# Optimization experiments

Measured on AMD Instinct MI355X. Metric: run time of the kernel, lower is better.

Reference implementation:

```python
import jax, jax.numpy as jnp
import numpy as np

SELECT_NUM = 5
N_OBJ = 256


def conv(x, w, b, stride=1, pad=None):
    """NCHW conv. pad=None -> VALID; pad=1 -> [(1,1),(1,1)]."""
    padding = 'VALID' if pad is None else [(pad, pad), (pad, pad)]
    out = jax.lax.conv_general_dilated(
        x, w, (stride, stride), padding,
        dimension_numbers=('NCHW', 'OIHW', 'NCHW'))
    return out + b[None, :, None, None]


def setup_inputs() -> dict:
    key = jax.random.key(0)
    ks = jax.random.split(key, 20)

    def p(k, shape, fan_in):
        return (jax.random.normal(k, shape, jnp.float32) / np.float32(np.sqrt(fan_in)))

    inp = {}
    inp['glob_feature'] = jax.random.normal(ks[0], (1, 1024, 28, 28), jnp.float32)
    inp['roi_features'] = jax.random.normal(ks[1], (N_OBJ, 2048, 7, 7), jnp.float32)
    # valid boxes in a 1280x720 image: x1>x0, y1>y0 so log(.) is finite
    x0 = jax.random.uniform(ks[2], (N_OBJ,), minval=0.0, maxval=600.0)
    y0 = jax.random.uniform(ks[3], (N_OBJ,), minval=0.0, maxval=340.0)
    x1 = x0 + jax.random.uniform(ks[4], (N_OBJ,), minval=10.0, maxval=600.0)
    y1 = y0 + jax.random.uniform(ks[5], (N_OBJ,), minval=10.0, maxval=340.0)
    inp['bbox'] = jnp.stack([x0, y0, x1, y1], axis=1)

    # global branch
    inp['w_glob1'] = p(ks[6], (512, 1024, 4, 4), 1024 * 16); inp['b_glob1'] = jnp.zeros(512, jnp.float32)
    inp['w_glob2'] = p(ks[7], (256, 512, 4, 4), 512 * 16);   inp['b_glob2'] = jnp.zeros(256, jnp.float32)
    # object branch
    inp['w_obj1'] = p(ks[8], (1024, 2048, 3, 3), 2048 * 9);  inp['b_obj1'] = jnp.zeros(1024, jnp.float32)
    inp['w_obj2'] = p(ks[9], (256, 1024, 3, 3), 1024 * 9);   inp['b_obj2'] = jnp.zeros(256, jnp.float32)
    # selector (516 = 260 obj + 256 glob)
    inp['w_sel1'] = p(ks[10], (256, 516, 3, 3), 516 * 9);    inp['b_sel1'] = jnp.zeros(256, jnp.float32)
    inp['w_sel2'] = p(ks[11], (16, 256, 3, 3), 256 * 9);     inp['b_sel2'] = jnp.zeros(16, jnp.float32)
    inp['w_sel3'] = p(ks[12], (1, 16, 3, 3), 16 * 9);        inp['b_sel3'] = jnp.zeros(1, jnp.float32)
    # FC head (eval mode: dropout = identity)
    inp['w_fc1'] = p(ks[13], (516, 256), 516);               inp['b_fc1'] = jnp.zeros(256, jnp.float32)
    inp['w_fc2'] = p(ks[14], (256 * SELECT_NUM, 64), 1280);  inp['b_fc2'] = jnp.zeros(64, jnp.float32)
    inp['w_fc3'] = p(ks[15], (64, 4), 64);                   inp['b_fc3'] = jnp.zeros(4, jnp.float32)
    return inp


def reference(glob_feature, roi_features, bbox,
              w_glob1, b_glob1, w_glob2, b_glob2,
              w_obj1, b_obj1, w_obj2, b_obj2,
              w_sel1, b_sel1, w_sel2, b_sel2, w_sel3, b_sel3,
              w_fc1, b_fc1, w_fc2, b_fc2, w_fc3, b_fc3):
    # global branch: [1,1024,28,28] -> [1,512,14,14] -> [1,256,7,7]; pool(7) is identity
    glob = jax.nn.relu(conv(glob_feature, w_glob1, b_glob1, stride=2, pad=1))
    glob = jax.nn.relu(conv(glob, w_glob2, b_glob2, stride=2, pad=1))

    # object branch: [N,2048,7,7] -> [N,1024,7,7] -> [N,256,7,7]
    obj = jax.nn.relu(conv(roi_features, w_obj1, b_obj1, pad=1))
    obj = jax.nn.relu(conv(obj, w_obj2, b_obj2, pad=1))

    # bbox normalization (uses original coords; image is 1280x720)
    x0, y0, x1, y1 = bbox[:, 0], bbox[:, 1], bbox[:, 2], bbox[:, 3]
    bb = jnp.stack([x0 / 1280.0, y0 / 720.0,
                    jnp.log(1280.0 / (x1 - x0)),
                    jnp.log(720.0 / (y1 - y0))], axis=1)  # [N,4]
    bb = jnp.broadcast_to(bb[:, :, None, None], (bb.shape[0], 4, 7, 7))
    obj = jnp.concatenate([bb, obj], axis=1)  # [N,260,7,7]

    # selector: concat with broadcast glob, 3 valid convs 7->5->3->1
    glob2 = jnp.broadcast_to(glob, (obj.shape[0], 256, 7, 7))
    s = jnp.concatenate([obj, glob2], axis=1)  # [N,516,7,7]
    s = jax.nn.relu(conv(s, w_sel1, b_sel1))
    s = jax.nn.relu(conv(s, w_sel2, b_sel2))
    s = conv(s, w_sel3, b_sel3).reshape(-1)  # [N]

    # top-k selection (sort descending over objects)
    idx = jnp.argsort(-s)[:SELECT_NUM]
    obj = obj[idx] / np.float32(SELECT_NUM)  # [5,260,7,7]

    # adaptive avg pool to 1x1 == mean over HW
    obj = obj.mean(axis=(2, 3))                               # [5,260]
    g = jnp.broadcast_to(glob.mean(axis=(2, 3)), (SELECT_NUM, 256))  # [5,256]
    x = jnp.concatenate([obj, g], axis=1)                     # [5,516]

    x = jax.nn.relu(x @ w_fc1 + b_fc1)   # dropout is identity in eval
    tmp = x.reshape(-1)                  # [1280]
    x = jax.nn.relu(tmp @ w_fc2 + b_fc2) # [64]
    x = x @ w_fc3 + b_fc3                # [4]
    return x
```

## Files before the change

kernel.cpp:

```cpp
#include <hip/hip_runtime.h>
#include <math.h>

using half8 = __attribute__((ext_vector_type(8))) _Float16;
using half4 = __attribute__((ext_vector_type(4))) _Float16;
using f32x4 = __attribute__((ext_vector_type(4))) float;

template<int CIN, int KC, int M_, int BM>
__global__ __launch_bounds__(256)
void transform_w(const float* __restrict__ w, _Float16* __restrict__ wt) {
  constexpr int NT = (KC / 32) * 9;
  __shared__ float lds[32 * 289];
  const int tid = threadIdx.x;
  const int s   = blockIdx.x;
  const int m0  = blockIdx.y * 32;
  const int ci0 = s * 32;
  int vlen = (CIN - ci0) * 9;
  if (vlen > 288) vlen = 288;
  if (vlen < 0) vlen = 0;

  for (int e = tid; e < 32 * 288; e += 256) {
    const int mi = e / 288, o = e - mi * 288;
    float v = 0.f;
    if (o < vlen) v = w[(size_t)(m0 + mi) * (CIN * 9) + (size_t)ci0 * 9 + o];
    lds[mi * 289 + o] = v;
  }
  __syncthreads();

  const int cc  = s >> 2;
  const int sub = s & 3;
  int ns = (KC - 128 * cc) / 32; if (ns > 4) ns = 4;
  const int mt = m0 / BM;
  const int mb = m0 - mt * BM;
  _Float16* base = wt + (size_t)mt * NT * (BM * 32);

  for (int u = tid; u < 36 * 256; u += 256) {
    const int chunk  = u >> 8;
    const int within = u & 255;
    const int g = chunk & 3, khkw = chunk >> 2;
    const int mi = within >> 3, i = within & 7;
    const int kt = 36 * cc + khkw * ns + sub;
    const float v = lds[mi * 289 + (8 * g + i) * 9 + khkw];
    base[(size_t)kt * (BM * 32) + g * (BM * 8) + (mb + mi) * 8 + i] = (_Float16)v;
  }
}

__global__ __launch_bounds__(256)
void convert_tr(const float* __restrict__ x, _Float16* __restrict__ xh) {
  __shared__ _Float16 t_s[49][136];
  const int tid   = threadIdx.x;
  const int cbase = blockIdx.x * 128;
  const int obj   = blockIdx.y;
  const float* src = x + (size_t)obj * 2048 * 49 + (size_t)cbase * 49;
  for (int e = tid; e < 128 * 49; e += 256) {
    const int ci = e / 49, pos = e - ci * 49;
    t_s[pos][ci] = (_Float16)src[e];
  }
  __syncthreads();
  _Float16* dst = xh + (size_t)obj * 49 * 2048 + cbase;
  for (int u = tid; u < 49 * 16; u += 256) {
    const int pos = u >> 4, l = u & 15;
    *(half8*)&dst[(size_t)pos * 2048 + l * 8] = *(const half8*)&t_s[pos][l * 8];
  }
}

template<int KC, int BM, int FN, int OHW, int PAD, bool TOUT, typename OUT_T,
         int NMT, int NOP>
__global__ __launch_bounds__(512)
void conv_mfma(const _Float16* __restrict__ Wt, const _Float16* __restrict__ X,
               const float* __restrict__ bias, OUT_T* __restrict__ out,
               int outc, int co_off) {
  constexpr int NT    = (KC / 32) * 9;
  constexpr int OPOS  = OHW * OHW;
  constexpr int WM    = BM / 4;
  constexpr int FR    = WM / 16;
  constexpr int CFULL = KC / 128;
  constexpr int TAIL  = KC - CFULL * 128;
  constexpr int NCH   = CFULL + (TAIL ? 1 : 0);

  __shared__ alignas(16) _Float16 x_s[2][50][136];

  const int tid  = threadIdx.x;
  const int wid  = tid >> 6;
  const int lane = tid & 63;
  const int g    = lane >> 4;
  const int ln   = lane & 15;
  const int obj  = wid >> 2;
  const int wm   = (wid & 3) * WM;

  const int bid = blockIdx.x;
  const int j = bid & 7, q = bid >> 3;
  constexpr int OPJ = 8 / NMT;
  const int mt = j / OPJ;
  const int op = (j % OPJ) * (NOP / OPJ) + q;

// ... 27 lines not shown
          const int row = u >> 4, l = u & 15;
          const int o = row >= 49 ? 1 : 0, pos = row - 49 * o;
          rg[v] = *(const half8*)(Xh + (size_t)(o * 49 + pos) * KC + cbase + l * 8);
        }
      }
    } else {
      if (tid < 392) {
        const int row = tid >> 2, l = tid & 3;
        const int o = row >= 49 ? 1 : 0, pos = row - 49 * o;
        rg[0] = *(const half8*)(Xh + (size_t)(o * 49 + pos) * KC + cbase + l * 8);
      }
    }
  };
  auto write_chunk = [&](int cw) {
    if (cw == 128) {
#pragma unroll
      for (int v = 0; v < 4; v++) {
        const int u = v * 512 + tid;
        if (u < 1568) {
          const int row = u >> 4, l = u & 15;
          const int o = row >= 49 ? 1 : 0, pos = row - 49 * o;
          *(half8*)&x_s[o][pos][l * 8] = rg[v];
        }
      }
    } else {
      if (tid < 392) {
        const int row = tid >> 2, l = tid & 3;
        const int o = row >= 49 ? 1 : 0, pos = row - 49 * o;
        *(half8*)&x_s[o][pos][l * 8] = rg[0];
      }
    }
  };

  const int afoff = (g * BM + wm + ln) * 8;
  const _Float16* ap = Wt + (size_t)mt * NT * (BM * 32) + afoff;
  half8 afA[FR], afB[FR], afC[FR];
#pragma unroll
  for (int r = 0; r < FR; r++) afA[r] = *(const half8*)(ap + r * 128);
  ap += BM * 32;
#pragma unroll
  for (int r = 0; r < FR; r++) afB[r] = *(const half8*)(ap + r * 128);
  ap += BM * 32;

  load_chunk(0, KC < 128 ? KC : 128);

  auto kstep = [&](half8 (&cur)[FR], half8 (&fut)[FR], int subbyte,
                   const int (&boff)[FN]) {
#pragma unroll
    for (int r = 0; r < FR; r++) fut[r] = *(const half8*)(ap + r * 128);
    ap += BM * 32;
    __builtin_amdgcn_s_setprio(1);
    const char* xb = (const char*)(&x_s[0][0][0]) + subbyte;
#pragma unroll
    for (int f = 0; f < FN; f++) {
      const half8 bf = *(const half8*)(xb + boff[f]);
#pragma unroll
      for (int r = 0; r < FR; r++)
        acc[r][f] = __builtin_amdgcn_mfma_f32_16x16x32_f16(cur[r], bf, acc[r][f], 0, 0, 0);
    }
    __builtin_amdgcn_s_setprio(0);
  };

  for (int c = 0; c < NCH; c++) {
    const int cw = (c < CFULL) ? 128 : TAIL;
    asm volatile("s_barrier" ::: "memory");
    write_chunk(cw);
    if (c + 1 < NCH)
      load_chunk((c + 1) * 128, (c + 1 < CFULL) ? 128 : TAIL);
    asm volatile("s_waitcnt lgkmcnt(0)\n\ts_barrier" ::: "memory");

    if (cw == 128) {
#pragma unroll
      for (int t9 = 0; t9 < 9; t9++) {
        const int kh = t9 / 3, kw = t9 - 3 * (t9 / 3);
        int boff[FN];
#pragma unroll
        for (int f = 0; f < FN; f++) {
          const int ih = ohv[f] + kh - PAD;
          const int iw = owv[f] + kw - PAD;
          bool v = pvv[f];
          if (PAD) v = v && ((unsigned)ih < 7u) && ((unsigned)iw < 7u);
          const int row = v ? (ih * 7 + iw) : 49;
          boff[f] = (obj * 50 * 136 + row * 136) * 2;
        }
#pragma unroll
        for (int s4 = 0; s4 < 4; s4++) {
          const int ph = (t9 * 4 + s4) % 3;
          const int subbyte = (s4 * 32 + 8 * g) * 2;
          if (ph == 0)      kstep(afA, afC, subbyte, boff);
          else if (ph == 1) kstep(afB, afA, subbyte, boff);
          else              kstep(afC, afB, subbyte, boff);
        }
      }
    } else {
#pragma unroll
      for (int t9 = 0; t9 < 9; t9++) {
        const int kh = t9 / 3, kw = t9 - 3 * (t9 / 3);
        int boff[FN];
#pragma unroll
        for (int f = 0; f < FN; f++) {
          const int ih = ohv[f] + kh - PAD;
          const int iw = owv[f] + kw - PAD;
          bool v = pvv[f];
          if (PAD) v = v && ((unsigned)ih < 7u) && ((unsigned)iw < 7u);
          const int row = v ? (ih * 7 + iw) : 49;
          boff[f] = (obj * 50 * 136 + row * 136) * 2;
        }
        const int ph = t9 % 3;
        const int subbyte = (8 * g) * 2;
        if (ph == 0)      kstep(afA, afC, subbyte, boff);
        else if (ph == 1) kstep(afB, afA, subbyte, boff);
        else              kstep(afC, afB, subbyte, boff);
      }
    }
  }

  if constexpr (TOUT) {
    __shared__ alignas(16) _Float16 ot_s[2][49][132];
    constexpr int PASSES = BM / 128;
#pragma unroll
    for (int p = 0; p < PASSES; p++) {
      if (p) asm volatile("s_barrier" ::: "memory");
      if (wm >= 128 * p && wm < 128 * (p + 1)) {
#pragma unroll
        for (int f = 0; f < FN; f++) {
          const int pos = ln + 16 * f;
          if (pos < OPOS) {
#pragma unroll
            for (int r = 0; r < FR; r++) {
              const int cl = wm - 128 * p + r * 16 + g * 4;
              half4 h;
#pragma unroll
              for (int e = 0; e < 4; e++)
                h[e] = (_Float16)fmaxf(
                    acc[r][f][e] + bias[mt * BM + wm + r * 16 + g * 4 + e], 0.f);
              *(half4*)&ot_s[obj][pos][cl] = h;
            }
          }
        }
      }
      asm volatile("s_waitcnt lgkmcnt(0)\n\ts_barrier" ::: "memory");
      _Float16* dst = (_Float16*)out;
      for (int u = tid; u < 2 * 49 * 32; u += 512) {
        const int row = u >> 5, l = u & 31;
        const int o = row >= 49 ? 1 : 0, pos = row - 49 * o;
        const half4 v = *(const half4*)&ot_s[o][pos][l * 4];
        *(half4*)&dst[((size_t)(2 * op + o) * OPOS + pos) * outc +
                      co_off + mt * BM + 128 * p + l * 4] = v;
      }
    }
  } else {
    const int bo = 2 * op + obj;
#pragma unroll
    for (int f = 0; f < FN; f++) {
      const int pos = ln + 16 * f;
      if (pos < OPOS) {
#pragma unroll
        for (int r = 0; r < FR; r++) {
          const int mrow = mt * BM + wm + r * 16 + g * 4;
#pragma unroll
          for (int e = 0; e < 4; e++) {
            const int m = mrow + e;
            float v = fmaxf(acc[r][f][e] + bias[m], 0.f);
            out[((size_t)bo * outc + co_off + m) * OPOS + pos] = (OUT_T)v;
          }
        }
      }
    }
  }
}

template<int M_, int CIN, int KH, int KW, int H, int W, int OH, int OW,
         int STRIDE, int PAD, int BATCH, int OUTC, int CO_OFF, bool RELU,
         int TM, int TN, int KSPLIT, bool PARTIAL>
__global__ __launch_bounds__(256)
void conv_gemm(const float* __restrict__ A,
               const float* __restrict__ X,
               const float* __restrict__ bias,
               float* __restrict__ out) {
  constexpr int K   = CIN * KH * KW;
  constexpr int N   = BATCH * OH * OW;
  constexpr int BK  = 16;
  constexpr int BM  = 16 * TM;
  constexpr int BN  = 16 * TN;
  constexpr int KCH = K / KSPLIT;

  __shared__ float a_s[BK][BM];
  __shared__ float b_s[BK][BN];

  const int t  = threadIdx.x;
  const int tx = t & 15;
  const int ty = t >> 4;
  const int n0 = blockIdx.x * BN;
  const int m0 = blockIdx.y * BM;
  const int kz = blockIdx.z;

  constexpr int AQ    = TM / 4;
  constexpr int TPR_A = 4 / AQ;
  const int am = t / TPR_A;
  const int ak = (t % TPR_A) * (4 * AQ);

  constexpr int BQ = TN / 4;
  const int bk = t & 15;
  const int bn = (t >> 4) * TN;

  float acc[TM][TN];
#pragma unroll
  for (int i = 0; i < TM; i++)
#pragma unroll
    for (int j = 0; j < TN; j++) acc[i][j] = 0.f;

  for (int k0 = kz * KCH; k0 < (kz + 1) * KCH; k0 += BK) {
    float4 av[AQ];
#pragma unroll
    for (int q = 0; q < AQ; q++) {
      av[q] = make_float4(0.f, 0.f, 0.f, 0.f);
      const int kq = k0 + ak + 4 * q;
      if ((m0 + am) < M_ && kq < K)
        av[q] = *reinterpret_cast<const float4*>(&A[(m0 + am) * K + kq]);
    }
    float bv[TN];
#pragma unroll
    for (int q = 0; q < TN; q++) bv[q] = 0.f;
    {
      const int kk = k0 + bk;
      if (kk < K) {
        const int ci = kk / (KH * KW);
        const int r  = kk - ci * (KH * KW);
        const int kh = r / KW;
        const int kw = r - kh * KW;
#pragma unroll
        for (int q = 0; q < TN; q++) {
          const int n = n0 + bn + q;
          if (n < N) {
            const int b   = n / (OH * OW);
            const int pos = n - b * (OH * OW);
            const int oh  = pos / OW;
            const int ow  = pos - oh * OW;
            const int ih  = oh * STRIDE - PAD + kh;
            const int iw  = ow * STRIDE - PAD + kw;
            if (ih >= 0 && ih < H && iw >= 0 && iw < W)
              bv[q] = X[((b * CIN + ci) * H + ih) * W + iw];
          }
        }
      }
    }
    __syncthreads();
#pragma unroll
    for (int q = 0; q < AQ; q++) {
      const int kq = ak + 4 * q;
      a_s[kq + 0][am] = av[q].x;
      a_s[kq + 1][am] = av[q].y;
      a_s[kq + 2][am] = av[q].z;
      a_s[kq + 3][am] = av[q].w;
    }
#pragma unroll
    for (int q = 0; q < BQ; q++)
      *reinterpret_cast<float4*>(&b_s[bk][bn + 4 * q]) =
          make_float4(bv[4 * q], bv[4 * q + 1], bv[4 * q + 2], bv[4 * q + 3]);
    __syncthreads();
#pragma unroll
    for (int kk2 = 0; kk2 < BK; kk2++) {
      float a[TM], b[TN];
#pragma unroll
      for (int q = 0; q < AQ; q++)
        *reinterpret_cast<float4*>(&a[4 * q]) =
            *reinterpret_cast<const float4*>(&a_s[kk2][ty * TM + 4 * q]);
#pragma unroll
      for (int q = 0; q < BQ; q++)
        *reinterpret_cast<float4*>(&b[4 * q]) =
            *reinterpret_cast<const float4*>(&b_s[kk2][tx * TN + 4 * q]);
#pragma unroll
      for (int i = 0; i < TM; i++)
#pragma unroll
        for (int j = 0; j < TN; j++)
          acc[i][j] = fmaf(a[i], b[j], acc[i][j]);
    }
  }

#pragma unroll
  for (int i = 0; i < TM; i++) {
    const int m = m0 + ty * TM + i;
    if (m < M_) {
#pragma unroll
      for (int j = 0; j < TN; j++) {
        const int n = n0 + tx * TN + j;
        if (n < N) {
          if (PARTIAL) {
            out[((size_t)kz * M_ + m) * N + n] = acc[i][j];
          } else {
            float v = acc[i][j] + bias[m];
            if (RELU) v = fmaxf(v, 0.f);
            const int b   = n / (OH * OW);
            const int pos = n - b * (OH * OW);
            out[(b * OUTC + CO_OFF + m) * (OH * OW) + pos] = v;
          }
        }
      }
    }
  }
}

__global__ void reduce_bias_relu(const float* __restrict__ part,
                                 const float* __restrict__ bias,
                                 float* __restrict__ out, int MN, int N, int KS) {
  const int e = blockIdx.x * 256 + threadIdx.x;
  if (e >= MN) return;
  float s = 0.f;
  for (int k = 0; k < KS; k++) s += part[(size_t)k * MN + e];
  s += bias[e / N];
  out[e] = fmaxf(s, 0.f);
}

__global__ __launch_bounds__(256)
void sel2_kernel(const float* __restrict__ x, const float* __restrict__ w,
                 const float* __restrict__ b, float* __restrict__ out) {
  const int wv   = (blockIdx.x * 256 + threadIdx.x) >> 6;
  const int lane = threadIdx.x & 63;
  const int obj  = wv >> 4, co = wv & 15;
  float acc[9];
#pragma unroll
  for (int p = 0; p < 9; p++) acc[p] = 0.f;
  const float* xo = x + (size_t)obj * 256 * 25;
  const float* wo = w + (size_t)co * 2304;
  for (int k = lane; k < 2304; k += 64) {
    const int ci = k / 9, rr = k - 9 * ci;
    const int kh = rr / 3, kw = rr - 3 * kh;
    const float wval = wo[k];
    const float* xc = xo + ci * 25;
#pragma unroll
    for (int oh = 0; oh < 3; oh++)
#pragma unroll
      for (int ow = 0; ow < 3; ow++)
        acc[oh * 3 + ow] = fmaf(xc[(oh + kh) * 5 + (ow + kw)], wval, acc[oh * 3 + ow]);
  }
  const float bv = b[co];
#pragma unroll
  for (int p = 0; p < 9; p++) {
    float v = acc[p];
#pragma unroll
    for (int off = 32; off; off >>= 1) v += __shfl_xor(v, off);
    if (lane == 0) out[(size_t)wv * 9 + p] = fmaxf(v + bv, 0.f);
  }
}

__global__ void prep_sin_t(const float* __restrict__ bbox,
                           const float* __restrict__ glob,
                           _Float16* __restrict__ sint) {
  const int b = blockIdx.x;
  const float x0 = bbox[b * 4 + 0], y0 = bbox[b * 4 + 1];
  const float x1 = bbox[b * 4 + 2], y1 = bbox[b * 4 + 3];
  const float bbv[4] = {x0 / 1280.f, y0 / 720.f,
                        logf(1280.f / (x1 - x0)), logf(720.f / (y1 - y0))};
  _Float16* base = sint + (size_t)b * 49 * 544;
  for (int e = threadIdx.x; e < 49 * 288; e += blockDim.x) {
    const int pos = e / 288, q = e - pos * 288;
    float v; int c;
    if (q < 4)        { v = bbv[q];                  c = q; }
    else if (q < 260) { v = glob[(q - 4) * 49 + pos]; c = q + 256; }
    else              { v = 0.f;                      c = q + 256; }
    base[pos * 544 + c] = (_Float16)v;
  }
}

__global__ void score_top5(const float* __restrict__ sel2,
                           const float* __restrict__ w3,
                           const float* __restrict__ b3,
                           int* __restrict__ idx_out) {
  __shared__ float w_s[144];
  __shared__ float s_s[256];
  const int t = threadIdx.x;
  if (t < 144) w_s[t] = w3[t];
  __syncthreads();
  float acc = b3[0];
  const float* p = sel2 + t * 144;
  for (int k = 0; k < 144; k++) acc += p[k] * w_s[k];
  s_s[t] = acc;
  __syncthreads();
  if (t == 0) {
    for (int i = 0; i < 5; i++) {
      float best = -1e30f;
      int bi = 0;
      for (int j = 0; j < 256; j++)
        if (s_s[j] > best) { best = s_s[j]; bi = j; }
      idx_out[i] = bi;
      s_s[bi] = -1e30f;
    }
  }
}

__global__ void pool_t(const _Float16* __restrict__ sint,
                       const float* __restrict__ glob,
                       const int* __restrict__ idx,
                       float* __restrict__ objsel,
                       float* __restrict__ g) {
  const int blk = blockIdx.x;
  const int t = threadIdx.x;
  if (blk < 5) {
    const int b = idx[blk];
    const _Float16* base = sint + (size_t)b * 49 * 544;
    for (int c = t; c < 260; c += blockDim.x) {
      float s = 0.f;
      for (int p = 0; p < 49; p++) s += (float)base[p * 544 + c];
      objsel[blk * 260 + c] = s * (1.f / 245.f);
    }
  } else {
    if (t < 256) {
      float s = 0.f;
      const float* p = glob + t * 49;
      for (int q = 0; q < 49; q++) s += p[q];
      g[t] = s * (1.f / 49.f);
    }
  }
}

__global__ void fc1_kernel(const float* __restrict__ objsel,
                           const float* __restrict__ g,
                           const float* __restrict__ w,
                           const float* __restrict__ b,
                           float* __restrict__ x1) {
  const int co = threadIdx.x;
  float acc[5];
#pragma unroll
  for (int i = 0; i < 5; i++) acc[i] = b[co];
  for (int k = 0; k < 260; k++) {
    const float wv = w[k * 256 + co];
#pragma unroll
    for (int i = 0; i < 5; i++) acc[i] = fmaf(objsel[i * 260 + k], wv, acc[i]);
  }
  for (int k = 260; k < 516; k++) {
    const float wv = w[k * 256 + co];
    const float gv = g[k - 260];
#pragma unroll
    for (int i = 0; i < 5; i++) acc[i] = fmaf(gv, wv, acc[i]);
  }
#pragma unroll
  for (int i = 0; i < 5; i++) x1[i * 256 + co] = fmaxf(acc[i], 0.f);
}

__global__ void fc23_kernel(const float* __restrict__ x1,
                            const float* __restrict__ w2,
                            const float* __restrict__ b2,
                            const float* __restrict__ w3,
                            const float* __restrict__ b3,
                            float* __restrict__ out) {
  __shared__ float x2[64];
  const int j = threadIdx.x;
  float acc = b2[j];
  for (int k = 0; k < 1280; k++) acc = fmaf(x1[k], w2[k * 64 + j], acc);
  x2[j] = fmaxf(acc, 0.f);
  __syncthreads();
  if (j < 4) {
    float a = b3[j];
    for (int k = 0; k < 64; k++) a = fmaf(x2[k], w3[k * 4 + j], a);
    out[j] = a;
  }
}

extern "C" void kernel_launch(void* const* d_in, const int* in_sizes, int n_in,
                              void* d_out, int out_size, void* d_ws, size_t ws_size,
                              hipStream_t stream) {
  (void)in_sizes; (void)n_in; (void)out_size; (void)ws_size;
  const float* glob_feature = (const float*)d_in[0];
  const float* roi          = (const float*)d_in[1];
  const float* bbox         = (const float*)d_in[2];
  const float* w_glob1      = (const float*)d_in[3];
  const float* b_glob1      = (const float*)d_in[4];
  const float* w_glob2      = (const float*)d_in[5];
  const float* b_glob2      = (const float*)d_in[6];
  const float* w_obj1       = (const float*)d_in[7];
  const float* b_obj1       = (const float*)d_in[8];
  const float* w_obj2       = (const float*)d_in[9];
  const float* b_obj2       = (const float*)d_in[10];
  const float* w_sel1       = (const float*)d_in[11];
  const float* b_sel1       = (const float*)d_in[12];
  const float* w_sel2       = (const float*)d_in[13];
  const float* b_sel2       = (const float*)d_in[14];
  const float* w_sel3       = (const float*)d_in[15];
  const float* b_sel3       = (const float*)d_in[16];
  const float* w_fc1        = (const float*)d_in[17];
  const float* b_fc1        = (const float*)d_in[18];
  const float* w_fc2        = (const float*)d_in[19];
  const float* b_fc2        = (const float*)d_in[20];
  const float* w_fc3        = (const float*)d_in[21];
  const float* b_fc3        = (const float*)d_in[22];

  float* ws = (float*)d_ws;
  _Float16* xh1     = (_Float16*)(ws);
  _Float16* wbuf1   = (_Float16*)(ws + 12845056);
  _Float16* obj1buf = (_Float16*)(ws + 22282240);
  _Float16* sint    = (_Float16*)(ws);
  _Float16* wbuf2   = (_Float16*)(ws + 3411968);
  _Float16* wbufs1  = (_Float16*)(ws + 4591616);
  float*    sel1buf = ws + 5218304;
  float*    glob1buf= ws + 6856704;
  float*    part1   = ws + 6957056;
  float*    part2   = ws + 8562688;
  float*    sel2buf = ws + 8763392;
  float*    globbuf = ws + 8800256;
  int*      idxbuf  = (int*)(ws + 8812800);
  float*    objsel  = ws + 8812808;
  float*    gbuf    = ws + 8814108;
  float*    x1buf   = ws + 8814364;

  transform_w<2048, 2048, 1024, 256><<<dim3(64, 32), 256, 0, stream>>>(w_obj1, wbuf1);
  convert_tr<<<dim3(16, 256), 256, 0, stream>>>(roi, xh1);
  conv_mfma<2048, 256, 4, 7, 1, true, _Float16, 4, 128>
      <<<dim3(512), 512, 0, stream>>>(wbuf1, xh1, b_obj1, obj1buf, 1024, 0);

  transform_w<1024, 1024, 256, 128><<<dim3(32, 8), 256, 0, stream>>>(w_obj2, wbuf2);
  transform_w<516, 544, 256, 128><<<dim3(17, 8), 256, 0, stream>>>(w_sel1, wbufs1);

  conv_gemm<512, 1024, 4, 4, 28, 28, 14, 14, 2, 1, 1, 512, 0, true, 4, 4, 16, true>
      <<<dim3(4, 8, 16), 256, 0, stream>>>(w_glob1, glob_feature, b_glob1, part1);
  reduce_bias_relu<<<dim3(392), 256, 0, stream>>>(part1, b_glob1, glob1buf, 100352, 196, 16);
  conv_gemm<256, 512, 4, 4, 14, 14, 7, 7, 2, 1, 1, 256, 0, true, 4, 4, 16, true>
      <<<dim3(1, 4, 16), 256, 0, stream>>>(w_glob2, glob1buf, b_glob2, part2);
  reduce_bias_relu<<<dim3(49), 256, 0, stream>>>(part2, b_glob2, globbuf, 12544, 49, 16);

  prep_sin_t<<<dim3(256), 256, 0, stream>>>(bbox, globbuf, sint);

  conv_mfma<1024, 128, 4, 7, 1, true, _Float16, 2, 128>
      <<<dim3(256), 512, 0, stream>>>(wbuf2, obj1buf, b_obj2, sint, 544, 4);
  conv_mfma<544, 128, 2, 5, 0, false, float, 2, 128>
      <<<dim3(256), 512, 0, stream>>>(wbufs1, sint, b_sel1, sel1buf, 256, 0);
  sel2_kernel<<<dim3(1024), 256, 0, stream>>>(sel1buf, w_sel2, b_sel2, sel2buf);
  score_top5<<<dim3(1), 256, 0, stream>>>(sel2buf, w_sel3, b_sel3, idxbuf);

  pool_t<<<dim3(6), 256, 0, stream>>>(sint, globbuf, idxbuf, objsel, gbuf);
  fc1_kernel<<<dim3(1), 256, 0, stream>>>(objsel, gbuf, w_fc1, b_fc1, x1buf);
  fc23_kernel<<<dim3(1), 64, 0, stream>>>(x1buf, w_fc2, b_fc2, w_fc3, b_fc3,
                                          (float*)d_out);
}
```

Baseline: 991.6 us.

## Merge prep kernels, retile obj1 conv with 8 waves, fuse FC head

Combines the weight transform and input transpose into one prep launch, and the obj2/sel1 weight transforms plus the glob1 conv into a second launch. It adds a new conv_mfma2 for the big obj1 conv with BM=512, 8 waves along M, and FN=7 covering both objects, so each block does more work. The score, top-5, pooling and FC layers are fused into one head kernel. This cuts launch overhead and is meant to improve weight reuse, at the cost of more registers per block and different occupancy.

```diff
diff --git a/kernel.cpp b/kernel.cpp
--- a/kernel.cpp
+++ b/kernel.cpp
@@ -6,18 +6,13 @@
 using f32x4 = __attribute__((ext_vector_type(4))) float;
 
 template<int CIN, int KC, int M_, int BM>
-__global__ __launch_bounds__(256)
-void transform_w(const float* __restrict__ w, _Float16* __restrict__ wt) {
+__device__ void transform_w_dev(float* lds, const float* __restrict__ w,
+                                _Float16* __restrict__ wt, int s, int m0, int tid) {
   constexpr int NT = (KC / 32) * 9;
-  __shared__ float lds[32 * 289];
-  const int tid = threadIdx.x;
-  const int s   = blockIdx.x;
-  const int m0  = blockIdx.y * 32;
   const int ci0 = s * 32;
   int vlen = (CIN - ci0) * 9;
   if (vlen > 288) vlen = 288;
   if (vlen < 0) vlen = 0;
-
   for (int e = tid; e < 32 * 288; e += 256) {
     const int mi = e / 288, o = e - mi * 288;
     float v = 0.f;
@@ -25,17 +20,13 @@
     lds[mi * 289 + o] = v;
   }
   __syncthreads();
-
-  const int cc  = s >> 2;
-  const int sub = s & 3;
+  const int cc = s >> 2, sub = s & 3;
   int ns = (KC - 128 * cc) / 32; if (ns > 4) ns = 4;
   const int mt = m0 / BM;
   const int mb = m0 - mt * BM;
   _Float16* base = wt + (size_t)mt * NT * (BM * 32);
-
   for (int u = tid; u < 36 * 256; u += 256) {
-    const int chunk  = u >> 8;
-    const int within = u & 255;
+    const int chunk = u >> 8, within = u & 255;
     const int g = chunk & 3, khkw = chunk >> 2;
     const int mi = within >> 3, i = within & 7;
     const int kt = 36 * cc + khkw * ns + sub;
@@ -44,12 +35,9 @@
   }
 }
 
-__global__ __launch_bounds__(256)
-void convert_tr(const float* __restrict__ x, _Float16* __restrict__ xh) {
-  __shared__ _Float16 t_s[49][136];
-  const int tid   = threadIdx.x;
-  const int cbase = blockIdx.x * 128;
-  const int obj   = blockIdx.y;
+__device__ void convert_tr_dev(_Float16 (*t_s)[136], const float* __restrict__ x,
+                               _Float16* __restrict__ xh, int cb, int obj, int tid) {
+  const int cbase = cb * 128;
   const float* src = x + (size_t)obj * 2048 * 49 + (size_t)cbase * 49;
   for (int e = tid; e < 128 * 49; e += 256) {
     const int ci = e / 49, pos = e - ci * 49;
@@ -60,6 +48,346 @@
   for (int u = tid; u < 49 * 16; u += 256) {
     const int pos = u >> 4, l = u & 15;
     *(half8*)&dst[(size_t)pos * 2048 + l * 8] = *(const half8*)&t_s[pos][l * 8];
+  }
+}
+
+template<int M_, int CIN, int KH, int KW, int H, int W, int OH, int OW,
+         int STRIDE, int PAD, int BATCH, int OUTC, int CO_OFF, bool RELU,
+         int TM, int TN, int KSPLIT, bool PARTIAL>
+__device__ void conv_gemm_dev(char* shraw, const float* __restrict__ A,
+                              const float* __restrict__ X,
+                              const float* __restrict__ bias,
+                              float* __restrict__ out,
+                              int n0, int m0, int kz, int t) {
+  constexpr int K   = CIN * KH * KW;
+  constexpr int N   = BATCH * OH * OW;
+  constexpr int BK  = 16;
+  constexpr int BM  = 16 * TM;
+  constexpr int BN  = 16 * TN;
+  constexpr int KCH = K / KSPLIT;
+
+  float (*a_s)[BM] = (float (*)[BM])shraw;
+  float (*b_s)[BN] = (float (*)[BN])(shraw + sizeof(float) * BK * BM);
+
+  const int tx = t & 15;
+  const int ty = t >> 4;
+  constexpr int AQ    = TM / 4;
+  constexpr int TPR_A = 4 / AQ;
+  const int am = t / TPR_A;
+  const int ak = (t % TPR_A) * (4 * AQ);
+  constexpr int BQ = TN / 4;
+  const int bk = t & 15;
+  const int bn = (t >> 4) * TN;
+
+  float acc[TM][TN];
+#pragma unroll
+  for (int i = 0; i < TM; i++)
+#pragma unroll
+    for (int j = 0; j < TN; j++) acc[i][j] = 0.f;
+
+  for (int k0 = kz * KCH; k0 < (kz + 1) * KCH; k0 += BK) {
+    float4 av[AQ];
+#pragma unroll
+    for (int q = 0; q < AQ; q++) {
+      av[q] = make_float4(0.f, 0.f, 0.f, 0.f);
+      const int kq = k0 + ak + 4 * q;
+      if ((m0 + am) < M_ && kq < K)
+        av[q] = *reinterpret_cast<const float4*>(&A[(m0 + am) * K + kq]);
+    }
+    float bv[TN];
+#pragma unroll
+    for (int q = 0; q < TN; q++) bv[q] = 0.f;
+    {
+      const int kk = k0 + bk;
+      if (kk < K) {
+        const int ci = kk / (KH * KW);
+        const int r  = kk - ci * (KH * KW);
+        const int kh = r / KW;
+        const int kw = r - kh * KW;
+#pragma unroll
+        for (int q = 0; q < TN; q++) {
+          const int n = n0 + bn + q;
+          if (n < N) {
+            const int b   = n / (OH * OW);
+            const int pos = n - b * (OH * OW);
+            const int oh  = pos / OW;
+            const int ow  = pos - oh * OW;
+            const int ih  = oh * STRIDE - PAD + kh;
+            const int iw  = ow * STRIDE - PAD + kw;
+            if (ih >= 0 && ih < H && iw >= 0 && iw < W)
+              bv[q] = X[((b * CIN + ci) * H + ih) * W + iw];
+          }
+        }
+      }
+    }
+    __syncthreads();
+#pragma unroll
+    for (int q = 0; q < AQ; q++) {
+      const int kq = ak + 4 * q;
+      a_s[kq + 0][am] = av[q].x;
+      a_s[kq + 1][am] = av[q].y;
+      a_s[kq + 2][am] = av[q].z;
+      a_s[kq + 3][am] = av[q].w;
+    }
+#pragma unroll
+    for (int q = 0; q < BQ; q++)
+      *reinterpret_cast<float4*>(&b_s[bk][bn + 4 * q]) =
+          make_float4(bv[4 * q], bv[4 * q + 1], bv[4 * q + 2], bv[4 * q + 3]);
+    __syncthreads();
+#pragma unroll
+    for (int kk2 = 0; kk2 < BK; kk2++) {
+      float a[TM], b[TN];
+#pragma unroll
+      for (int q = 0; q < AQ; q++)
+        *reinterpret_cast<float4*>(&a[4 * q]) =
+            *reinterpret_cast<const float4*>(&a_s[kk2][ty * TM + 4 * q]);
+#pragma unroll
+      for (int q = 0; q < BQ; q++)
+        *reinterpret_cast<float4*>(&b[4 * q]) =
+            *reinterpret_cast<const float4*>(&b_s[kk2][tx * TN + 4 * q]);
+#pragma unroll
+      for (int i = 0; i < TM; i++)
+#pragma unroll
+        for (int j = 0; j < TN; j++)
+          acc[i][j] = fmaf(a[i], b[j], acc[i][j]);
+    }
+  }
+
+#pragma unroll
+  for (int i = 0; i < TM; i++) {
+    const int m = m0 + ty * TM + i;
+    if (m < M_) {
+#pragma unroll
+      for (int j = 0; j < TN; j++) {
+        const int n = n0 + tx * TN + j;
+        if (n < N) {
+          if (PARTIAL) {
+            out[((size_t)kz * M_ + m) * N + n] = acc[i][j];
+          } else {
+            float v = acc[i][j] + bias[m];
+            if (RELU) v = fmaxf(v, 0.f);
+            const int b   = n / (OH * OW);
+            const int pos = n - b * (OH * OW);
+            out[(b * OUTC + CO_OFF + m) * (OH * OW) + pos] = v;
+          }
+        }
+      }
+    }
+  }
+}
+
+template<int M_, int CIN, int KH, int KW, int H, int W, int OH, int OW,
+         int STRIDE, int PAD, int BATCH, int OUTC, int CO_OFF, bool RELU,
+         int TM, int TN, int KSPLIT, bool PARTIAL>
+__global__ __launch_bounds__(256)
+void conv_gemm(const float* __restrict__ A, const float* __restrict__ X,
+               const float* __restrict__ bias, float* __restrict__ out) {
+  __shared__ char sh[16 * (16 * TM + 16 * TN) * 4];
+  conv_gemm_dev<M_, CIN, KH, KW, H, W, OH, OW, STRIDE, PAD, BATCH, OUTC, CO_OFF,
+                RELU, TM, TN, KSPLIT, PARTIAL>(
+      sh, A, X, bias, out, blockIdx.x * 16 * TN, blockIdx.y * 16 * TM,
+      blockIdx.z, threadIdx.x);
+}
+
+__global__ __launch_bounds__(256)
+void prep1(const float* __restrict__ w_obj1, _Float16* __restrict__ wbuf1,
+           const float* __restrict__ roi, _Float16* __restrict__ xh1) {
+  __shared__ char sh[32 * 289 * 4];
+  int b = blockIdx.x;
+  if (b < 2048) {
+    transform_w_dev<2048, 2048, 1024, 512>((float*)sh, w_obj1, wbuf1,
+                                           b & 63, (b >> 6) * 32, threadIdx.x);
+  } else {
+    b -= 2048;
+    convert_tr_dev((_Float16(*)[136])sh, roi, xh1, b & 15, b >> 4, threadIdx.x);
+  }
+}
+
+__global__ __launch_bounds__(256)
+void prep2(const float* __restrict__ w_obj2, _Float16* __restrict__ wbuf2,
+           const float* __restrict__ w_sel1, _Float16* __restrict__ wbufs1,
+           const float* __restrict__ w_glob1, const float* __restrict__ gfeat,
+           float* __restrict__ part1) {
+  __shared__ char sh[32 * 289 * 4];
+  int b = blockIdx.x;
+  if (b < 256) {
+    transform_w_dev<1024, 1024, 256, 128>((float*)sh, w_obj2, wbuf2,
+                                          b & 31, (b >> 5) * 32, threadIdx.x);
+  } else if (b < 392) {
+    b -= 256;
+    transform_w_dev<516, 544, 256, 128>((float*)sh, w_sel1, wbufs1,
+                                        b % 17, (b / 17) * 32, threadIdx.x);
+  } else {
+    b -= 392;
+    conv_gemm_dev<512, 1024, 4, 4, 28, 28, 14, 14, 2, 1, 1, 512, 0, true,
+                  4, 4, 16, true>(sh, w_glob1, gfeat, nullptr, part1,
+                                  (b & 3) * 64, ((b >> 2) & 7) * 64, b >> 5,
+                                  threadIdx.x);
+  }
+}
+
+template<int KC, int BM, int FN, int OHW, int PAD, int NMT, int NOP>
+__global__ __launch_bounds__(512)
+void conv_mfma2(const _Float16* __restrict__ Wt, const _Float16* __restrict__ X,
+                const float* __restrict__ bias, _Float16* __restrict__ out,
+                int outc, int co_off) {
+  constexpr int NT   = (KC / 32) * 9;
+  constexpr int OPOS = OHW * OHW;
+  constexpr int WM   = BM / 8;
+  constexpr int FR   = WM / 16;
+  constexpr int NCH  = KC / 128;
+
+  __shared__ alignas(16) _Float16 x_s[2][50][136];
+
+  const int tid  = threadIdx.x;
+  const int wid  = tid >> 6;
+  const int lane = tid & 63;
+  const int g    = lane >> 4;
+  const int ln   = lane & 15;
+  const int wm   = wid * WM;
+
+  const int bid = blockIdx.x;
+  const int j = bid & 7, q = bid >> 3;
+  constexpr int OPJ = 8 / NMT;
+  const int mt = j / OPJ;
+  const int op = (j % OPJ) * (NOP / OPJ) + q;
+
+  if (tid < 272) x_s[tid / 136][49][tid % 136] = (_Float16)0.f;
+
+  int ohv[FN], owv[FN], objv[FN];
+  bool pvv[FN];
+#pragma unroll
+  for (int f = 0; f < FN; f++) {
+    const int p = ln + 16 * f;
+    pvv[f] = p < 2 * OPOS;
+    const int ob = pvv[f] ? (p / OPOS) : 1;
+    objv[f] = ob;
+    const int pp = pvv[f] ? (p - ob * OPOS) : 0;
+    ohv[f] = pp / OHW;
+    owv[f] = pp % OHW;
+  }
+
+  f32x4 acc[FR][FN];
+#pragma unroll
+  for (int r = 0; r < FR; r++)
+#pragma unroll
+    for (int f = 0; f < FN; f++) acc[r][f] = (f32x4){0.f, 0.f, 0.f, 0.f};
+
+  const _Float16* Xh = X + (size_t)(2 * op) * 49 * KC;
+
+  half8 rg[4];
+  auto load_chunk = [&](int cbase) {
+#pragma unroll
+    for (int v = 0; v < 4; v++) {
+      const int u = v * 512 + tid;
+      if (u < 1568) {
+        const int row = u >> 4, l = u & 15;
+        const int o = row >= 49 ? 1 : 0, pos = row - 49 * o;
+        rg[v] = *(const half8*)(Xh + (size_t)(o * 49 + pos) * KC + cbase + l * 8);
+      }
+    }
+  };
+  auto write_chunk = [&]() {
+#pragma unroll
+    for (int v = 0; v < 4; v++) {
+      const int u = v * 512 + tid;
+      if (u < 1568) {
+        const int row = u >> 4, l = u & 15;
+        const int o = row >= 49 ? 1 : 0, pos = row - 49 * o;
+        *(half8*)&x_s[o][pos][l * 8] = rg[v];
+      }
+    }
+  };
+
+  const _Float16* ap = Wt + (size_t)mt * NT * (BM * 32) + (g * BM + wm + ln) * 8;
+  half8 afA[FR], afB[FR], afC[FR];
+#pragma unroll
+  for (int r = 0; r < FR; r++) afA[r] = *(const half8*)(ap + r * 128);
+  ap += BM * 32;
+#pragma unroll
+  for (int r = 0; r < FR; r++) afB[r] = *(const half8*)(ap + r * 128);
+  ap += BM * 32;
+
+  load_chunk(0);
+
+  auto kstep = [&](half8 (&cur)[FR], half8 (&fut)[FR], int subbyte,
+                   const int (&boff)[FN]) {
+#pragma unroll
+    for (int r = 0; r < FR; r++) fut[r] = *(const half8*)(ap + r * 128);
+    ap += BM * 32;
+    __builtin_amdgcn_s_setprio(1);
+    const char* xb = (const char*)(&x_s[0][0][0]) + subbyte;
+#pragma unroll
+    for (int f = 0; f < FN; f++) {
+      const half8 bf = *(const half8*)(xb + boff[f]);
+#pragma unroll
+      for (int r = 0; r < FR; r++)
+        acc[r][f] = __builtin_amdgcn_mfma_f32_16x16x32_f16(cur[r], bf, acc[r][f], 0, 0, 0);
+    }
+    __builtin_amdgcn_s_setprio(0);
+  };
+
+  for (int c = 0; c < NCH; c++) {
+    asm volatile("s_barrier" ::: "memory");
+    write_chunk();
+    if (c + 1 < NCH) load_chunk((c + 1) * 128);
+    asm volatile("s_waitcnt lgkmcnt(0)\n\ts_barrier" ::: "memory");
+#pragma unroll
+    for (int t9 = 0; t9 < 9; t9++) {
+      const int kh = t9 / 3, kw = t9 - 3 * (t9 / 3);
+      int boff[FN];
+#pragma unroll
+      for (int f = 0; f < FN; f++) {
+        const int ih = ohv[f] + kh - PAD;
+        const int iw = owv[f] + kw - PAD;
+        bool v = pvv[f];
+        if (PAD) v = v && ((unsigned)ih < 7u) && ((unsigned)iw < 7u);
+        const int row = v ? (ih * 7 + iw) : 49;
+        boff[f] = (objv[f] * 50 * 136 + row * 136) * 2;
+      }
+#pragma unroll
+      for (int s4 = 0; s4 < 4; s4++) {
+        const int ph = (t9 * 4 + s4) % 3;
+        const int subbyte = (s4 * 32 + 8 * g) * 2;
+        if (ph == 0)      kstep(afA, afC, subbyte, boff);
+        else if (ph == 1) kstep(afB, afA, subbyte, boff);
+        else              kstep(afC, afB, subbyte, boff);
+      }
+    }
+  }
+
+  _Float16 (*ot_s)[49][132] = (_Float16 (*)[49][132]) & x_s[0][0][0];
+  constexpr int PASSES = BM / 128;
+#pragma unroll
+  for (int p = 0; p < PASSES; p++) {
+    asm volatile("s_waitcnt lgkmcnt(0)\n\ts_barrier" ::: "memory");
+    if (wm >= 128 * p && wm < 128 * (p + 1)) {
+#pragma unroll
+      for (int f = 0; f < FN; f++) {
+        if (pvv[f]) {
+          const int pos = ohv[f] * OHW + owv[f];
+          const int ob  = objv[f];
+#pragma unroll
+          for (int r = 0; r < FR; r++) {
+            const int cl = wm - 128 * p + r * 16 + g * 4;
+            half4 h;
+#pragma unroll
+            for (int e = 0; e < 4; e++)
+              h[e] = (_Float16)fmaxf(
+                  acc[r][f][e] + bias[mt * BM + wm + r * 16 + g * 4 + e], 0.f);
+            *(half4*)&ot_s[ob][pos][cl] = h;
+          }
+        }
+      }
+    }
+    asm volatile("s_waitcnt lgkmcnt(0)\n\ts_barrier" ::: "memory");
+    for (int u = tid; u < 2 * OPOS * 32; u += 512) {
+      const int row = u >> 5, l = u & 31;
+      const int o = row >= OPOS ? 1 : 0, pos = row - OPOS * o;
+      const half4 v = *(const half4*)&ot_s[o][pos][l * 4];
+      *(half4*)&out[((size_t)(2 * op + o) * OPOS + pos) * outc + co_off +
+                    mt * BM + 128 * p + l * 4] = v;
+    }
   }
 }
 
@@ -153,8 +481,7 @@
     }
   };
 
-  const int afoff = (g * BM + wm + ln) * 8;
-  const _Float16* ap = Wt + (size_t)mt * NT * (BM * 32) + afoff;
+  const _Float16* ap = Wt + (size_t)mt * NT * (BM * 32) + (g * BM + wm + ln) * 8;
   half8 afA[FR], afB[FR], afC[FR];
 #pragma unroll
   for (int r = 0; r < FR; r++) afA[r] = *(const half8*)(ap + r * 128);
@@ -182,6 +509,7 @@
     __builtin_amdgcn_s_setprio(0);
   };
 
+  int ktile = 0;
   for (int c = 0; c < NCH; c++) {
     const int cw = (c < CFULL) ? 128 : TAIL;
     asm volatile("s_barrier" ::: "memory");
@@ -189,86 +517,57 @@
     if (c + 1 < NCH)
       load_chunk((c + 1) * 128, (c + 1 < CFULL) ? 128 : TAIL);
     asm volatile("s_waitcnt lgkmcnt(0)\n\ts_barrier" ::: "memory");
-
-    if (cw == 128) {
-#pragma unroll
-      for (int t9 = 0; t9 < 9; t9++) {
-        const int kh = t9 / 3, kw = t9 - 3 * (t9 / 3);
-        int boff[FN];
-#pragma unroll
-        for (int f = 0; f < FN; f++) {
-          const int ih = ohv[f] + kh - PAD;
-          const int iw = owv[f] + kw - PAD;
-          bool v = pvv[f];
-          if (PAD) v = v && ((unsigned)ih < 7u) && ((unsigned)iw < 7u);
-          const int row = v ? (ih * 7 + iw) : 49;
-          boff[f] = (obj * 50 * 136 + row * 136) * 2;
-        }
-#pragma unroll
-        for (int s4 = 0; s4 < 4; s4++) {
-          const int ph = (t9 * 4 + s4) % 3;
-          const int subbyte = (s4 * 32 + 8 * g) * 2;
-          if (ph == 0)      kstep(afA, afC, subbyte, boff);
-          else if (ph == 1) kstep(afB, afA, subbyte, boff);
-          else              kstep(afC, afB, subbyte, boff);
-        }
-      }
-    } else {
-#pragma unroll
-      for (int t9 = 0; t9 < 9; t9++) {
-        const int kh = t9 / 3, kw = t9 - 3 * (t9 / 3);
-        int boff[FN];
-#pragma unroll
-        for (int f = 0; f < FN; f++) {
-          const int ih = ohv[f] + kh - PAD;
-          const int iw = owv[f] + kw - PAD;
-          bool v = pvv[f];
-          if (PAD) v = v && ((unsigned)ih < 7u) && ((unsigned)iw < 7u);
-          const int row = v ? (ih * 7 + iw) : 49;
-          boff[f] = (obj * 50 * 136 + row * 136) * 2;
-        }
-        const int ph = t9 % 3;
-        const int subbyte = (8 * g) * 2;
+    const int nsub = cw / 32;
+    for (int khkw = 0; khkw < 9; khkw++) {
+      const int kh = khkw / 3, kw = khkw - 3 * (khkw / 3);
+      int boff[FN];
+#pragma unroll
+      for (int f = 0; f < FN; f++) {
+        const int ih = ohv[f] + kh - PAD;
+        const int iw = owv[f] + kw - PAD;
+        bool v = pvv[f];
+        if (PAD) v = v && ((unsigned)ih < 7u) && ((unsigned)iw < 7u);
+        const int row = v ? (ih * 7 + iw) : 49;
+        boff[f] = (obj * 50 * 136 + row * 136) * 2;
+      }
+      for (int sub = 0; sub < nsub; sub++) {
+        const int ph = ktile % 3;
+        const int subbyte = (sub * 32 + 8 * g) * 2;
         if (ph == 0)      kstep(afA, afC, subbyte, boff);
         else if (ph == 1) kstep(afB, afA, subbyte, boff);
         else              kstep(afC, afB, subbyte, boff);
+        ktile++;
       }
     }
   }
 
   if constexpr (TOUT) {
-    __shared__ alignas(16) _Float16 ot_s[2][49][132];
-    constexpr int PASSES = BM / 128;
-#pragma unroll
-    for (int p = 0; p < PASSES; p++) {
-      if (p) asm volatile("s_barrier" ::: "memory");
-      if (wm >= 128 * p && wm < 128 * (p + 1)) {
-#pragma unroll
-        for (int f = 0; f < FN; f++) {
-          const int pos = ln + 16 * f;
-          if (pos < OPOS) {
-#pragma unroll
-            for (int r = 0; r < FR; r++) {
-              const int cl = wm - 128 * p + r * 16 + g * 4;
-              half4 h;
-#pragma unroll
-              for (int e = 0; e < 4; e++)
-                h[e] = (_Float16)fmaxf(
-                    acc[r][f][e] + bias[mt * BM + wm + r * 16 + g * 4 + e], 0.f);
-              *(half4*)&ot_s[obj][pos][cl] = h;
-            }
-          }
+    _Float16 (*ot_s)[49][132] = (_Float16 (*)[49][132]) & x_s[0][0][0];
+    asm volatile("s_waitcnt lgkmcnt(0)\n\ts_barrier" ::: "memory");
+#pragma unroll
+    for (int f = 0; f < FN; f++) {
+      const int pos = ln + 16 * f;
+      if (pos < OPOS) {
+#pragma unroll
+        for (int r = 0; r < FR; r++) {
+          const int cl = wm + r * 16 + g * 4;
+          half4 h;
+#pragma unroll
+          for (int e = 0; e < 4; e++)
+            h[e] = (_Float16)fmaxf(
+                acc[r][f][e] + bias[mt * BM + wm + r * 16 + g * 4 + e], 0.f);
+          *(half4*)&ot_s[obj][pos][cl] = h;
         }
       }
-      asm volatile("s_waitcnt lgkmcnt(0)\n\ts_barrier" ::: "memory");
-      _Float16* dst = (_Float16*)out;
-      for (int u = tid; u < 2 * 49 * 32; u += 512) {
-        const int row = u >> 5, l = u & 31;
-        const int o = row >= 49 ? 1 : 0, pos = row - 49 * o;
-        const half4 v = *(const half4*)&ot_s[o][pos][l * 4];
-        *(half4*)&dst[((size_t)(2 * op + o) * OPOS + pos) * outc +
-                      co_off + mt * BM + 128 * p + l * 4] = v;
-      }
+    }
+    asm volatile("s_waitcnt lgkmcnt(0)\n\ts_barrier" ::: "memory");
+    _Float16* dst = (_Float16*)out;
+    for (int u = tid; u < 2 * OPOS * 32; u += 512) {
+      const int row = u >> 5, l = u & 31;
+      const int o = row >= OPOS ? 1 : 0, pos = row - OPOS * o;
+      const half4 v = *(const half4*)&ot_s[o][pos][l * 4];
+      *(half4*)&dst[((size_t)(2 * op + o) * OPOS + pos) * outc + co_off +
+                    mt * BM + l * 4] = v;
     }
   } else {
     const int bo = 2 * op + obj;
@@ -284,137 +583,6 @@
             const int m = mrow + e;
             float v = fmaxf(acc[r][f][e] + bias[m], 0.f);
             out[((size_t)bo * outc + co_off + m) * OPOS + pos] = (OUT_T)v;
-          }
-        }
-      }
-    }
-  }
-}
-
-template<int M_, int CIN, int KH, int KW, int H, int W, int OH, int OW,
-         int STRIDE, int PAD, int BATCH, int OUTC, int CO_OFF, bool RELU,
-         int TM, int TN, int KSPLIT, bool PARTIAL>
-__global__ __launch_bounds__(256)
-void conv_gemm(const float* __restrict__ A,
-               const float* __restrict__ X,
-               const float* __restrict__ bias,
-               float* __restrict__ out) {
-  constexpr int K   = CIN * KH * KW;
-  constexpr int N   = BATCH * OH * OW;
-  constexpr int BK  = 16;
-  constexpr int BM  = 16 * TM;
-  constexpr int BN  = 16 * TN;
-  constexpr int KCH = K / KSPLIT;
-
-  __shared__ float a_s[BK][BM];
-  __shared__ float b_s[BK][BN];
-
-  const int t  = threadIdx.x;
-  const int tx = t & 15;
-  const int ty = t >> 4;
-  const int n0 = blockIdx.x * BN;
-  const int m0 = blockIdx.y * BM;
-  const int kz = blockIdx.z;
-
-  constexpr int AQ    = TM / 4;
-  constexpr int TPR_A = 4 / AQ;
-  const int am = t / TPR_A;
-  const int ak = (t % TPR_A) * (4 * AQ);
-
-  constexpr int BQ = TN / 4;
-  const int bk = t & 15;
-  const int bn = (t >> 4) * TN;
-
-  float acc[TM][TN];
-#pragma unroll
-  for (int i = 0; i < TM; i++)
-#pragma unroll
-    for (int j = 0; j < TN; j++) acc[i][j] = 0.f;
-
-  for (int k0 = kz * KCH; k0 < (kz + 1) * KCH; k0 += BK) {
-    float4 av[AQ];
-#pragma unroll
-    for (int q = 0; q < AQ; q++) {
-      av[q] = make_float4(0.f, 0.f, 0.f, 0.f);
-      const int kq = k0 + ak + 4 * q;
-      if ((m0 + am) < M_ && kq < K)
-        av[q] = *reinterpret_cast<const float4*>(&A[(m0 + am) * K + kq]);
-    }
-    float bv[TN];
-#pragma unroll
-    for (int q = 0; q < TN; q++) bv[q] = 0.f;
-    {
-      const int kk = k0 + bk;
-      if (kk < K) {
-        const int ci = kk / (KH * KW);
-        const int r  = kk - ci * (KH * KW);
-        const int kh = r / KW;
-        const int kw = r - kh * KW;
-#pragma unroll
-        for (int q = 0; q < TN; q++) {
-          const int n = n0 + bn + q;
-          if (n < N) {
-            const int b   = n / (OH * OW);
-            const int pos = n - b * (OH * OW);
-            const int oh  = pos / OW;
-            const int ow  = pos - oh * OW;
-            const int ih  = oh * STRIDE - PAD + kh;
-            const int iw  = ow * STRIDE - PAD + kw;
-            if (ih >= 0 && ih < H && iw >= 0 && iw < W)
-              bv[q] = X[((b * CIN + ci) * H + ih) * W + iw];
-          }
-        }
-      }
-    }
-    __syncthreads();
-#pragma unroll
-    for (int q = 0; q < AQ; q++) {
-      const int kq = ak + 4 * q;
-      a_s[kq + 0][am] = av[q].x;
-      a_s[kq + 1][am] = av[q].y;
-      a_s[kq + 2][am] = av[q].z;
-      a_s[kq + 3][am] = av[q].w;
-    }
-#pragma unroll
-    for (int q = 0; q < BQ; q++)
-      *reinterpret_cast<float4*>(&b_s[bk][bn + 4 * q]) =
-          make_float4(bv[4 * q], bv[4 * q + 1], bv[4 * q + 2], bv[4 * q + 3]);
-    __syncthreads();
-#pragma unroll
-    for (int kk2 = 0; kk2 < BK; kk2++) {
-      float a[TM], b[TN];
-#pragma unroll
-      for (int q = 0; q < AQ; q++)
-        *reinterpret_cast<float4*>(&a[4 * q]) =
-            *reinterpret_cast<const float4*>(&a_s[kk2][ty * TM + 4 * q]);
-#pragma unroll
-      for (int q = 0; q < BQ; q++)
-        *reinterpret_cast<float4*>(&b[4 * q]) =
-            *reinterpret_cast<const float4*>(&b_s[kk2][tx * TN + 4 * q]);
-#pragma unroll
-      for (int i = 0; i < TM; i++)
-#pragma unroll
-        for (int j = 0; j < TN; j++)
-          acc[i][j] = fmaf(a[i], b[j], acc[i][j]);
-    }
-  }
-
-#pragma unroll
-  for (int i = 0; i < TM; i++) {
-    const int m = m0 + ty * TM + i;
-    if (m < M_) {
-#pragma unroll
-      for (int j = 0; j < TN; j++) {
-        const int n = n0 + tx * TN + j;
-        if (n < N) {
-          if (PARTIAL) {
-            out[((size_t)kz * M_ + m) * N + n] = acc[i][j];
-          } else {
-            float v = acc[i][j] + bias[m];
-            if (RELU) v = fmaxf(v, 0.f);
-            const int b   = n / (OH * OW);
-            const int pos = n - b * (OH * OW);
-            out[(b * OUTC + CO_OFF + m) * (OH * OW) + pos] = v;
           }
         }
       }
@@ -477,104 +645,90 @@
   for (int e = threadIdx.x; e < 49 * 288; e += blockDim.x) {
     const int pos = e / 288, q = e - pos * 288;
     float v; int c;
-    if (q < 4)        { v = bbv[q];                  c = q; }
+    if (q < 4)        { v = bbv[q];                   c = q; }
     else if (q < 260) { v = glob[(q - 4) * 49 + pos]; c = q + 256; }
     else              { v = 0.f;                      c = q + 256; }
     base[pos * 544 + c] = (_Float16)v;
   }
 }
 
-__global__ void score_top5(const float* __restrict__ sel2,
-                           const float* __restrict__ w3,
-                           const float* __restrict__ b3,
-                           int* __restrict__ idx_out) {
-  __shared__ float w_s[144];
+__global__ __launch_bounds__(512)
+void head_kernel(const float* __restrict__ sel2, const float* __restrict__ w3,
+                 const float* __restrict__ b3, const _Float16* __restrict__ sint,
+                 const float* __restrict__ glob, const float* __restrict__ w1,
+                 const float* __restrict__ b1, const float* __restrict__ w2,
+                 const float* __restrict__ b2, const float* __restrict__ wf3,
+                 const float* __restrict__ bf3, float* __restrict__ out) {
+  __shared__ float w3_s[144];
   __shared__ float s_s[256];
+  __shared__ int   idx_s[5];
+  __shared__ float objsel_s[5 * 260];
+  __shared__ float g_s[256];
+  __shared__ float x1_s[1280];
+  __shared__ float x2_s[64];
   const int t = threadIdx.x;
-  if (t < 144) w_s[t] = w3[t];
+  if (t < 144) w3_s[t] = w3[t];
   __syncthreads();
-  float acc = b3[0];
-  const float* p = sel2 + t * 144;
-  for (int k = 0; k < 144; k++) acc += p[k] * w_s[k];
-  s_s[t] = acc;
+  if (t < 256) {
+    float acc = b3[0];
+    const float* p = sel2 + t * 144;
+    for (int k = 0; k < 144; k++) acc += p[k] * w3_s[k];
+    s_s[t] = acc;
+  } else {
+    const int c = t - 256;
+    float s = 0.f;
+    const float* p = glob + c * 49;
+    for (int q = 0; q < 49; q++) s += p[q];
+    g_s[c] = s * (1.f / 49.f);
+  }
   __syncthreads();
   if (t == 0) {
     for (int i = 0; i < 5; i++) {
-      float best = -1e30f;
-      int bi = 0;
+      float best = -1e30f; int bi = 0;
       for (int j = 0; j < 256; j++)
         if (s_s[j] > best) { best = s_s[j]; bi = j; }
-      idx_out[i] = bi;
+      idx_s[i] = bi;
       s_s[bi] = -1e30f;
     }
   }
-}
-
-__global__ void pool_t(const _Float16* __restrict__ sint,
-                       const float* __restrict__ glob,
-                       const int* __restrict__ idx,
-                       float* __restrict__ objsel,
-                       float* __restrict__ g) {
-  const int blk = blockIdx.x;
-  const int t = threadIdx.x;
-  if (blk < 5) {
-    const int b = idx[blk];
-    const _Float16* base = sint + (size_t)b * 49 * 544;
-    for (int c = t; c < 260; c += blockDim.x) {
-      float s = 0.f;
-      for (int p = 0; p < 49; p++) s += (float)base[p * 544 + c];
-      objsel[blk * 260 + c] = s * (1.f / 245.f);
-    }
-  } else {
-    if (t < 256) {
-      float s = 0.f;
-      const float* p = glob + t * 49;
-      for (int q = 0; q < 49; q++) s += p[q];
-      g[t] = s * (1.f / 49.f);
-    }
-  }
-}
-
-__global__ void fc1_kernel(const float* __restrict__ objsel,
-                           const float* __restrict__ g,
-                           const float* __restrict__ w,
-                           const float* __restrict__ b,
-                           float* __restrict__ x1) {
-  const int co = threadIdx.x;
-  float acc[5];
-#pragma unroll
-  for (int i = 0; i < 5; i++) acc[i] = b[co];
-  for (int k = 0; k < 260; k++) {
-    const float wv = w[k * 256 + co];
-#pragma unroll
-    for (int i = 0; i < 5; i++) acc[i] = fmaf(objsel[i * 260 + k], wv, acc[i]);
-  }
-  for (int k = 260; k < 516; k++) {
-    const float wv = w[k * 256 + co];
-    const float gv = g[k - 260];
-#pragma unroll
-    for (int i = 0; i < 5; i++) acc[i] = fmaf(gv, wv, acc[i]);
-  }
-#pragma unroll
-  for (int i = 0; i < 5; i++) x1[i * 256 + co] = fmaxf(acc[i], 0.f);
-}
-
-__global__ void fc23_kernel(const float* __restrict__ x1,
-                            const float* __restrict__ w2,
-                            const float* __restrict__ b2,
-                            const float* __restrict__ w3,
-                            const float* __restrict__ b3,
-                            float* __restrict__ out) {
-  __shared__ float x2[64];
-  const int j = threadIdx.x;
-  float acc = b2[j];
-  for (int k = 0; k < 1280; k++) acc = fmaf(x1[k], w2[k * 64 + j], acc);
-  x2[j] = fmaxf(acc, 0.f);
   __syncthreads();
-  if (j < 4) {
-    float a = b3[j];
-    for (int k = 0; k < 64; k++) a = fmaf(x2[k], w3[k * 4 + j], a);
-    out[j] = a;
+  for (int e = t; e < 5 * 260; e += 512) {
+    const int i = e / 260, c = e - 260 * i;
+    const _Float16* base = sint + (size_t)idx_s[i] * 49 * 544;
+    float s = 0.f;
+    for (int p = 0; p < 49; p++) s += (float)base[p * 544 + c];
+    objsel_s[e] = s * (1.f / 245.f);
+  }
+  __syncthreads();
+  if (t < 256) {
+    float acc[5];
+#pragma unroll
+    for (int i = 0; i < 5; i++) acc[i] = b1[t];
+    for (int k = 0; k < 260; k++) {
+      const float wv = w1[k * 256 + t];
+#pragma unroll
+      for (int i = 0; i < 5; i++) acc[i] = fmaf(objsel_s[i * 260 + k], wv, acc[i]);
+    }
+    for (int k = 260; k < 516; k++) {
+      const float wv = w1[k * 256 + t];
+      const float gv = g_s[k - 260];
+#pragma unroll
+      for (int i = 0; i < 5; i++) acc[i] = fmaf(gv, wv, acc[i]);
+    }
+#pragma unroll
+    for (int i = 0; i < 5; i++) x1_s[i * 256 + t] = fmaxf(acc[i], 0.f);
+  }
+  __syncthreads();
+  if (t < 64) {
+    float a = b2[t];
+    for (int k = 0; k < 1280; k++) a = fmaf(x1_s[k], w2[k * 64 + t], a);
+    x2_s[t] = fmaxf(a, 0.f);
+  }
+  __syncthreads();
+  if (t < 4) {
+    float a = bf3[t];
+    for (int k = 0; k < 64; k++) a = fmaf(x2_s[k], wf3[k * 4 + t], a);
+    out[t] = a;
   }
 }
 
@@ -619,37 +773,23 @@
   float*    part2   = ws + 8562688;
   float*    sel2buf = ws + 8763392;
   float*    globbuf = ws + 8800256;
-  int*      idxbuf  = (int*)(ws + 8812800);
-  float*    objsel  = ws + 8812808;
-  float*    gbuf    = ws + 8814108;
-  float*    x1buf   = ws + 8814364;
-
-  transform_w<2048, 2048, 1024, 256><<<dim3(64, 32), 256, 0, stream>>>(w_obj1, wbuf1);
-  convert_tr<<<dim3(16, 256), 256, 0, stream>>>(roi, xh1);
-  conv_mfma<2048, 256, 4, 7, 1, true, _Float16, 4, 128>
-      <<<dim3(512), 512, 0, stream>>>(wbuf1, xh1, b_obj1, obj1buf, 1024, 0);
-
-  transform_w<1024, 1024, 256, 128><<<dim3(32, 8), 256, 0, stream>>>(w_obj2, wbuf2);
-  transform_w<516, 544, 256, 128><<<dim3(17, 8), 256, 0, stream>>>(w_sel1, wbufs1);
-
-  conv_gemm<512, 1024, 4, 4, 28, 28, 14, 14, 2, 1, 1, 512, 0, true, 4, 4, 16, true>
-      <<<dim3(4, 8, 16), 256, 0, stream>>>(w_glob1, glob_feature, b_glob1, part1);
+
+  prep1<<<dim3(6144), 256, 0, stream>>>(w_obj1, wbuf1, roi, xh1);
+  conv_mfma2<2048, 512, 7, 7, 1, 2, 128>
+      <<<dim3(256), 512, 0, stream>>>(wbuf1, xh1, b_obj1, obj1buf, 1024, 0);
+  prep2<<<dim3(904), 256, 0, stream>>>(w_obj2, wbuf2, w_sel1, wbufs1,
+                                       w_glob1, glob_feature, part1);
   reduce_bias_relu<<<dim3(392), 256, 0, stream>>>(part1, b_glob1, glob1buf, 100352, 196, 16);
   conv_gemm<256, 512, 4, 4, 14, 14, 7, 7, 2, 1, 1, 256, 0, true, 4, 4, 16, true>
       <<<dim3(1, 4, 16), 256, 0, stream>>>(w_glob2, glob1buf, b_glob2, part2);
   reduce_bias_relu<<<dim3(49), 256, 0, stream>>>(part2, b_glob2, globbuf, 12544, 49, 16);
-
   prep_sin_t<<<dim3(256), 256, 0, stream>>>(bbox, globbuf, sint);
-
   conv_mfma<1024, 128, 4, 7, 1, true, _Float16, 2, 128>
       <<<dim3(256), 512, 0, stream>>>(wbuf2, obj1buf, b_obj2, sint, 544, 4);
   conv_mfma<544, 128, 2, 5, 0, false, float, 2, 128>
       <<<dim3(256), 512, 0, stream>>>(wbufs1, sint, b_sel1, sel1buf, 256, 0);
   sel2_kernel<<<dim3(1024), 256, 0, stream>>>(sel1buf, w_sel2, b_sel2, sel2buf);
-  score_top5<<<dim3(1), 256, 0, stream>>>(sel2buf, w_sel3, b_sel3, idxbuf);
-
-  pool_t<<<dim3(6), 256, 0, stream>>>(sint, globbuf, idxbuf, objsel, gbuf);
-  fc1_kernel<<<dim3(1), 256, 0, stream>>>(objsel, gbuf, w_fc1, b_fc1, x1buf);
-  fc23_kernel<<<dim3(1), 64, 0, stream>>>(x1buf, w_fc2, b_fc2, w_fc3, b_fc3,
-                                          (float*)d_out);
-}
+  head_kernel<<<dim3(1), 512, 0, stream>>>(sel2buf, w_sel3, b_sel3, sint,
+                                           globbuf, w_fc1, b_fc1, w_fc2, b_fc2,
+                                           w_fc3, b_fc3, (float*)d_out);
+}
```

Result: no change. 1.008 ms (+1.7%).
